# Kernel optimization log

Measured on AMD Instinct MI355X. Metric: run time of the kernel, lower is better.

Reference implementation:

```python
import jax, jax.numpy as jnp
import numpy as np

N = 50000   # nodes
F = 128     # v_feats
K = 128     # filters
H = 3       # multi_head
M = 10      # fixed neighbor count (hardcoded repeat(1,10,1) in source)


def setup_inputs() -> dict:
    key = jax.random.key(0)
    ks = jax.random.split(key, 10)
    vertices = jax.random.normal(ks[0], (N, F), jnp.float32)
    nh_indices = jax.random.randint(ks[1], (N, M), 0, N)
    int_indices = jax.random.randint(ks[2], (N, M), 0, N)
    nh_edges = jax.random.uniform(ks[3], (N, M), jnp.float32)
    int_edges = jax.random.uniform(ks[4], (N, M), jnp.float32)
    is_int = jax.random.randint(ks[5], (N,), 0, 2)
    scale = 0.05
    Wvc = jax.random.normal(ks[6], (H, F, K), jnp.float32) * scale
    Wvn_int = jax.random.normal(ks[7], (H, F, K), jnp.float32) * scale
    Wvn_nh = jax.random.normal(ks[8], (H, F, K), jnp.float32) * scale
    a = jax.random.normal(ks[9], (H, 2 * K, 1), jnp.float32) * scale
    bv = jnp.zeros((H, K), jnp.float32)
    return dict(vertices=vertices, nh_indices=nh_indices, int_indices=int_indices,
                nh_edges=nh_edges, int_edges=int_edges, is_int=is_int,
                Wvc=Wvc, bv=bv, Wvn_int=Wvn_int, Wvn_nh=Wvn_nh, a=a)


def reference(vertices, nh_indices, int_indices, nh_edges, int_edges, is_int,
              Wvc, bv, Wvn_int, Wvn_nh, a):
    n = vertices.shape[0]
    k = a.shape[1] // 2
    # Project center and neighbor features for all heads at once.
    Zc = jnp.einsum('nf,hfk->hnk', vertices, Wvc)        # [H,N,K]
    Vint = jnp.einsum('nf,hfk->hnk', vertices, Wvn_int)  # [H,N,K]
    Vnh = jnp.einsum('nf,hfk->hnk', vertices, Wvn_nh)    # [H,N,K]
    # cat((neighbor, center)) @ a  ==  neighbor @ a[:k] + center @ a[k:]
    a_n = a[:, :k, 0]  # [H,K]
    a_c = a[:, k:, 0]  # [H,K]
    e_center = jnp.einsum('hnk,hk->hn', Zc, a_c)[:, :, None]  # [H,N,1]

    def branch(Vside, idx, edges):
        mask = (idx != -1).astype(vertices.dtype)           # [N,M], -1 = pad
        g = Vside[:, idx]                                   # [H,N,M,K] gather
        e = jnp.einsum('hnmk,hk->hnm', g, a_n) + e_center   # [H,N,M]
        # faithful to source: scores zeroed (not -inf) by mask/edges before softmax
        e = e * mask[None] * edges[None]
        alpha = jax.nn.softmax(e, axis=2)                   # [H,N,M]
        norm = jnp.maximum(mask.sum(axis=1), 1.0)           # [N]
        Zn = jnp.einsum('hnmk,hnm->hnk', g * mask[None, :, :, None], alpha)
        return Zn / norm[None, :, None]

    Zn_inter = branch(Vint, int_indices, int_edges)
    Zn_chain = branch(Vnh, nh_indices, nh_edges)
    z = jax.nn.relu(Zc + Zn_inter + Zn_chain + bv[:, None, :])  # [H,N,K]
    # torch.cat(head outputs, dim=1) -> [N, H*K]
    return jnp.transpose(z, (1, 0, 2)).reshape(n, -1)
```

## Files before the change

kernel.cpp:

```cpp
#include <hip/hip_runtime.h>
#include <stdint.h>

#define N_V 50000
#define F_DIM 128
#define K_DIM 128
#define H_DIM 3
#define M_DIM 10
#define TILES_PER_BLK 4

using bf16x8 = __attribute__((ext_vector_type(8))) short;
using f32x4  = __attribute__((ext_vector_type(4))) float;

__device__ inline unsigned short f2bf(float f) {
    union { float f; uint32_t u; } v; v.f = f;
    uint32_t u = v.u;
    u += 0x7fffu + ((u >> 16) & 1u);
    return (unsigned short)(u >> 16);
}

#define LDS_AS __attribute__((address_space(3)))
__device__ inline void gl2lds16(const void* g, void* l) {
    __builtin_amdgcn_global_load_lds(
        (const __attribute__((address_space(1))) unsigned int*)g,
        (LDS_AS unsigned int*)l, 16, 0, 0);
}

#define WTOT (9 * 128 * 128)
#define XCH  (N_V * 16)
#define WACT (9 * 128)

__global__ void prep(const float* __restrict__ Wvc,
                     const float* __restrict__ Wvn_int,
                     const float* __restrict__ Wvn_nh,
                     const float* __restrict__ X,
                     const float* __restrict__ a,
                     unsigned short* __restrict__ Wt,
                     unsigned short* __restrict__ Xb,
                     unsigned short* __restrict__ wab) {
    int idx = blockIdx.x * 256 + threadIdx.x;
    if (idx < WTOT) {
        int b   = idx >> 14;
        int rem = idx & 16383;
        int k = rem >> 7;
        int f = rem & 127;
        int h = b / 3, t = b - 3 * h;
        const float* src = (t == 0) ? Wvc : (t == 1) ? Wvn_int : Wvn_nh;
        Wt[idx] = f2bf(src[(h * 128 + f) * 128 + k]);
        return;
    }
    int xi = idx - WTOT;
    if (xi < XCH) {
        const float4* Xv = (const float4*)X;
        float4 v0 = Xv[xi * 2];
        float4 v1 = Xv[xi * 2 + 1];
        uint4 o;
        o.x = (uint32_t)f2bf(v0.x) | ((uint32_t)f2bf(v0.y) << 16);
        o.y = (uint32_t)f2bf(v0.z) | ((uint32_t)f2bf(v0.w) << 16);
        o.z = (uint32_t)f2bf(v1.x) | ((uint32_t)f2bf(v1.y) << 16);
        o.w = (uint32_t)f2bf(v1.z) | ((uint32_t)f2bf(v1.w) << 16);
        *(uint4*)&Xb[(size_t)xi * 8] = o;
        return;
    }
    int wi = xi - XCH;
    if (wi < WACT) {
        int b = wi >> 7, f = wi & 127;
        int h = b / 3, t = b - 3 * h;
        const float* src = (t == 0) ? Wvc : (t == 1) ? Wvn_int : Wvn_nh;
        const float4* wrow = (const float4*)&src[(h * 128 + f) * 128];
        const float4* av   = (const float4*)&a[h * 256 + (t == 0 ? 128 : 0)];
        float acc = 0.f;
        #pragma unroll 8
        for (int c = 0; c < 32; ++c) {
            float4 w = wrow[c], x = av[c];
            acc += w.x * x.x + w.y * x.y + w.z * x.z + w.w * x.w;
        }
        wab[b * 128 + f] = f2bf(acc);
    }
}

__global__ __launch_bounds__(256, 3) void gemm_kernel(
    const unsigned short* __restrict__ Xb,
    const unsigned short* __restrict__ Wt,
    const unsigned short* __restrict__ wab,
    float* __restrict__ out,
    uint8_t* __restrict__ Vint,
    uint8_t* __restrict__ Vnh,
    float* __restrict__ ec4,
    float* __restrict__ ei4,
    float* __restrict__ en4) {
    __shared__ unsigned short As[2][64 * 128];

    const int tid  = threadIdx.x;
    const int b    = blockIdx.y;
    const int hh   = b / 3;
    const int tt   = b - 3 * hh;
    const int wv   = tid >> 6;
    const int lane = tid & 63;
    const int q    = lane >> 4;
    const int ln   = lane & 15;
    const int cb   = (wv >> 1) * 64;
    const int rb   = (wv & 1) * 32;
    const int m0   = blockIdx.x * (64 * TILES_PER_BLK);

    auto stage = [&](int buf, int tile) {
        const int mb = m0 + tile * 64;
        #pragma unroll
        for (int it = 0; it < 4; ++it) {
            int c16 = it * 256 + tid;
            int r   = c16 >> 4;
            int p   = c16 & 15;
            int lch = p ^ (r & 15);
            int gr  = mb + r;
            if (gr >= N_V) gr = 0;
            gl2lds16(Xb + (size_t)gr * 128 + lch * 8, &As[buf][c16 * 8]);
        }
    };

    stage(0, 0);

    const unsigned short* Wb = Wt + (size_t)b * 16384;
    bf16x8 bfr[4][4];
    #pragma unroll
    for (int ct = 0; ct < 4; ++ct) {
        int col = cb + 4 * ln + ct;
        #pragma unroll
        for (int kk = 0; kk < 4; ++kk)
            bfr[ct][kk] = *(const bf16x8*)&Wb[col * 128 + kk * 32 + q * 8];
    }

    const bool do_e = (b == 0) && (wv < 2);
    bf16x8 wz[4];
    if (do_e) {
        #pragma unroll
        for (int kk = 0; kk < 4; ++kk) {
            bf16x8 z = {0, 0, 0, 0, 0, 0, 0, 0};
            if (ln < 9) z = *(const bf16x8*)&wab[ln * 128 + kk * 32 + q * 8];
            wz[kk] = z;
        }
    }

    __syncthreads();

    const int c0 = cb + 4 * ln;
    #pragma unroll
    for (int t = 0; t < TILES_PER_BLK; ++t) {
        const int mb = m0 + t * 64;

        if (t + 1 < TILES_PER_BLK) stage((t + 1) & 1, t + 1);

        bf16x8 afr[2][4];
        #pragma unroll
        for (int rt = 0; rt < 2; ++rt) {
            int r = rb + rt * 16 + ln;
            #pragma unroll
            for (int kk = 0; kk < 4; ++kk) {
                int p = (kk * 4 + q) ^ ln;
                afr[rt][kk] = *(const bf16x8*)&As[t & 1][r * 128 + p * 8];
            }
        }

        f32x4 acc[2][4];
        #pragma unroll
        for (int rt = 0; rt < 2; ++rt)
            #pragma unroll
            for (int ct = 0; ct < 4; ++ct) acc[rt][ct] = (f32x4){0.f, 0.f, 0.f, 0.f};

        #pragma unroll
        for (int rt = 0; rt < 2; ++rt)
            #pragma unroll
            for (int kk = 0; kk < 4; ++kk)
                #pragma unroll
                for (int ct = 0; ct < 4; ++ct)
                    acc[rt][ct] = __builtin_amdgcn_mfma_f32_16x16x32_bf16(
                        afr[rt][kk], bfr[ct][kk], acc[rt][ct], 0, 0, 0);

        if (do_e) {
            #pragma unroll
            for (int rt = 0; rt < 2; ++rt) {
                f32x4 ae = (f32x4){0.f, 0.f, 0.f, 0.f};
                #pragma unroll
                for (int kk = 0; kk < 4; ++kk)
                    ae = __builtin_amdgcn_mfma_f32_16x16x32_bf16(
                        afr[rt][kk], wz[kk], ae, 0, 0, 0);
                if (ln < 9) {
                    int h2 = ln / 3, t2 = ln - 3 * h2;
                    float* ep = (t2 == 0) ? ec4 : (t2 == 1) ? ei4 : en4;
                    #pragma unroll
                    for (int rg = 0; rg < 4; ++rg) {
                        int gr = mb + rb + rt * 16 + q * 4 + rg;
                        if (gr < N_V) ep[gr * 4 + h2] = ae[rg];
                    }
                }
            }
        }

        __syncthreads();

        if (tt == 0) {
            #pragma unroll
            for (int rt = 0; rt < 2; ++rt)
                #pragma unroll
                for (int rg = 0; rg < 4; ++rg) {
                    int gr = mb + rb + rt * 16 + q * 4 + rg;
                    if (gr >= N_V) continue;
                    float4 v = make_float4(acc[rt][0][rg], acc[rt][1][rg],
                                           acc[rt][2][rg], acc[rt][3][rg]);
                    *(float4*)&out[(size_t)gr * 384 + hh * 128 + c0] = v;
                }
        } else {
            uint8_t* Vside = (tt == 1) ? Vint : Vnh;
            #pragma unroll
            for (int rt = 0; rt < 2; ++rt)
                #pragma unroll
                for (int rg = 0; rg < 4; ++rg) {
                    int gr = mb + rb + rt * 16 + q * 4 + rg;
                    if (gr >= N_V) continue;
                    int pk = __builtin_amdgcn_cvt_pk_fp8_f32(
                        acc[rt][0][rg], acc[rt][1][rg], 0, false);
                    pk = __builtin_amdgcn_cvt_pk_fp8_f32(
                        acc[rt][2][rg], acc[rt][3][rg], pk, true);
                    *(uint32_t*)&Vside[((size_t)(hh * N_V + gr)) * 128 + c0] =
                        (uint32_t)pk;
                }
        }
    }
}

__global__ __launch_bounds__(256) void attn_kernel(
    const int* __restrict__ nh_idx, const int* __restrict__ int_idx,
    const float* __restrict__ nh_edge, const float* __restrict__ int_edge,
    const float* __restrict__ bv,
    const uint8_t* __restrict__ Vint,
    const uint8_t* __restrict__ Vnh,
    const float* __restrict__ ec4, const float* __restrict__ ei4,
    const float* __restrict__ en4,
    float* __restrict__ out) {
    const int wv   = threadIdx.x >> 6;
    const int lane = threadIdx.x & 63;
    const int n    = blockIdx.x * 4 + wv;
    if (n >= N_V) return;
    const int g  = lane >> 4;
    const int gl = lane & 15;

    const bool part = (g <= 1) && (gl < M_DIM);
    int jm = -1; float wm = 0.f;
    if (part) {
        const int*   idx = (g == 0) ? int_idx  : nh_idx;
        const float* ed  = (g == 0) ? int_edge : nh_edge;
        jm = idx[n * M_DIM + gl];
        wm = ed[n * M_DIM + gl];
    }
    const bool  valid = part && (jm >= 0);
    const int   jc    = valid ? jm : 0;
    const float vfl   = valid ? 1.f : 0.f;

    float cf = vfl;
    #pragma unroll
    for (int off = 1; off < 16; off <<= 1) cf += __shfl_xor(cf, off, 64);
    const float cnorm = fmaxf(cf, 1.f);

    const int src_base = (g < 2 ? 0 : 16) + (g & 1) * 5;
    int jrow[5];
    #pragma unroll
    for (int i = 0; i < 5; ++i) jrow[i] = __shfl(jc, src_base + i, 64);

    uint2 pv[3][5];
    #pragma unroll
    for (int h = 0; h < H_DIM; ++h) {
        const uint8_t* Vb = ((g < 2) ? Vint : Vnh) + (size_t)h * N_V * 128;
        #pragma unroll
        for (int i = 0; i < 5; ++i)
            pv[h][i] = *(const uint2*)&Vb[(size_t)jrow[i] * 128 + gl * 8];
    }
    float4 ev = make_float4(0.f, 0.f, 0.f, 0.f);
    if (part) ev = *(const float4*)&(((g == 0) ? ei4 : en4)[jc * 4]);
    const float4 ecv = *(const float4*)&ec4[n * 4];

    float4 zc[3], bb[3];
    if (g < 2) {
        #pragma unroll
        for (int h = 0; h < H_DIM; ++h) {
            zc[h] = *(const float4*)&out[(size_t)n * 384 + h * 128 + gl * 8 + g * 4];
            bb[h] = *(const float4*)&bv[h * 128 + gl * 8 + g * 4];
        }
    }

    #pragma unroll
    for (int h = 0; h < H_DIM; ++h) {
        const float eh  = (h == 0) ? ev.x  : (h == 1) ? ev.y  : ev.z;
        const float ech = (h == 0) ? ecv.x : (h == 1) ? ecv.y : ecv.z;

        float l = -3.0e38f;
        if (part) l = valid ? (eh + ech) * wm : 0.f;
        float mx = l;
        #pragma unroll
        for (int off = 1; off < 16; off <<= 1) mx = fmaxf(mx, __shfl_xor(mx, off, 64));
        float ex = part ? __expf(l - mx) : 0.f;
        float sv = ex;
        #pragma unroll
        for (int off = 1; off < 16; off <<= 1) sv += __shfl_xor(sv, off, 64);
        float alphap = valid ? ex / (sv * cnorm) : 0.f;

        float acc[8] = {0.f, 0.f, 0.f, 0.f, 0.f, 0.f, 0.f, 0.f};
        #pragma unroll
        for (int i = 0; i < 5; ++i) {
            float al = __shfl(alphap, src_base + i, 64);
            uint2 p  = pv[h][i];
            auto f01 = __builtin_amdgcn_cvt_pk_f32_fp8(p.x, false);
            auto f23 = __builtin_amdgcn_cvt_pk_f32_fp8(p.x, true);
            auto f45 = __builtin_amdgcn_cvt_pk_f32_fp8(p.y, false);
            auto f67 = __builtin_amdgcn_cvt_pk_f32_fp8(p.y, true);
            acc[0] += al * f01[0];
            acc[1] += al * f01[1];
            acc[2] += al * f23[0];
            acc[3] += al * f23[1];
            acc[4] += al * f45[0];
            acc[5] += al * f45[1];
            acc[6] += al * f67[0];
            acc[7] += al * f67[1];
        }
        #pragma unroll
        for (int c = 0; c < 8; ++c) {
            acc[c] += __shfl_xor(acc[c], 16, 64);
            acc[c] += __shfl_xor(acc[c], 32, 64);
        }
        if (g < 2) {
            size_t o = (size_t)n * 384 + h * 128 + gl * 8 + g * 4;
            float4 zn;
            if (g == 0) zn = make_float4(acc[0], acc[1], acc[2], acc[3]);
            else        zn = make_float4(acc[4], acc[5], acc[6], acc[7]);
            float4 r;
            r.x = fmaxf(zc[h].x + zn.x + bb[h].x, 0.f);
            r.y = fmaxf(zc[h].y + zn.y + bb[h].y, 0.f);
            r.z = fmaxf(zc[h].z + zn.z + bb[h].z, 0.f);
            r.w = fmaxf(zc[h].w + zn.w + bb[h].w, 0.f);
            *(float4*)&out[o] = r;
        }
    }
}

extern "C" void kernel_launch(void* const* d_in, const int* in_sizes, int n_in,
                              void* d_out, int out_size, void* d_ws, size_t ws_size,
                              hipStream_t stream) {
    const float* vertices    = (const float*)d_in[0];
    const int*   nh_indices  = (const int*)d_in[1];
    const int*   int_indices = (const int*)d_in[2];
    const float* nh_edges    = (const float*)d_in[3];
    const float* int_edges   = (const float*)d_in[4];
    const float* Wvc     = (const float*)d_in[6];
    const float* bv      = (const float*)d_in[7];
    const float* Wvn_int = (const float*)d_in[8];
    const float* Wvn_nh  = (const float*)d_in[9];
    const float* a       = (const float*)d_in[10];
    float* out = (float*)d_out;

    char* ws = (char*)d_ws;
    size_t off = 0;
    unsigned short* Wt = (unsigned short*)(ws + off);
    off += (size_t)WTOT * 2;                  off = (off + 255) & ~(size_t)255;
    unsigned short* wab = (unsigned short*)(ws + off);
    off += (size_t)WACT * 2;                  off = (off + 255) & ~(size_t)255;
    unsigned short* Xb = (unsigned short*)(ws + off);
    off += (size_t)N_V * 128 * 2;             off = (off + 255) & ~(size_t)255;
    uint8_t* Vint = (uint8_t*)(ws + off);
    off += (size_t)H_DIM * N_V * 128;         off = (off + 255) & ~(size_t)255;
    uint8_t* Vnh = (uint8_t*)(ws + off);
    off += (size_t)H_DIM * N_V * 128;         off = (off + 255) & ~(size_t)255;
    float* ec4 = (float*)(ws + off);
    off += (size_t)N_V * 4 * 4;               off = (off + 255) & ~(size_t)255;
    float* ei4 = (float*)(ws + off);
    off += (size_t)N_V * 4 * 4;               off = (off + 255) & ~(size_t)255;
    float* en4 = (float*)(ws + off);
    off += (size_t)N_V * 4 * 4;

    int prep_threads = WTOT + XCH + WACT;
    prep<<<(prep_threads + 255) / 256, 256, 0, stream>>>(
        Wvc, Wvn_int, Wvn_nh, vertices, a, Wt, Xb, wab);

    dim3 grid_g((N_V + 64 * TILES_PER_BLK - 1) / (64 * TILES_PER_BLK), 9);
    gemm_kernel<<<grid_g, 256, 0, stream>>>(Xb, Wt, wab, out, Vint, Vnh,
                                            ec4, ei4, en4);

    attn_kernel<<<(N_V + 3) / 4, 256, 0, stream>>>(
        nh_indices, int_indices, nh_edges, int_edges, bv,
        Vint, Vnh, ec4, ei4, en4, out);
}
```

Before: 246.1 us.

## Store center projection in fp16, interleave heads in V layout, drop softmax max

The GEMM now writes the center projection Zc to a separate fp16 buffer instead of fp32 into the output, which halves the write and later read traffic. The fp8 neighbor projections switch to a node-major layout with all three heads contiguous, so each gathered neighbor row is one 384-byte region instead of three scattered rows. The softmax max-subtraction reduction is removed, relying on the small logit range. Risks are lower precision for Zc and possible overflow of exp if the logits grow.

```diff
diff --git a/kernel.cpp b/kernel.cpp
--- a/kernel.cpp
+++ b/kernel.cpp
@@ -10,12 +10,19 @@
 
 using bf16x8 = __attribute__((ext_vector_type(8))) short;
 using f32x4  = __attribute__((ext_vector_type(4))) float;
+using h4     = __attribute__((ext_vector_type(4))) _Float16;
 
 __device__ inline unsigned short f2bf(float f) {
     union { float f; uint32_t u; } v; v.f = f;
     uint32_t u = v.u;
     u += 0x7fffu + ((u >> 16) & 1u);
     return (unsigned short)(u >> 16);
+}
+
+__device__ inline uint32_t pkh2(float a, float b) {
+    union { _Float16 h[2]; uint32_t u; } v;
+    v.h[0] = (_Float16)a; v.h[1] = (_Float16)b;
+    return v.u;
 }
 
 #define LDS_AS __attribute__((address_space(3)))
@@ -82,7 +89,7 @@
     const unsigned short* __restrict__ Xb,
     const unsigned short* __restrict__ Wt,
     const unsigned short* __restrict__ wab,
-    float* __restrict__ out,
+    _Float16* __restrict__ zc16,
     uint8_t* __restrict__ Vint,
     uint8_t* __restrict__ Vnh,
     float* __restrict__ ec4,
@@ -203,9 +210,10 @@
                 for (int rg = 0; rg < 4; ++rg) {
                     int gr = mb + rb + rt * 16 + q * 4 + rg;
                     if (gr >= N_V) continue;
-                    float4 v = make_float4(acc[rt][0][rg], acc[rt][1][rg],
-                                           acc[rt][2][rg], acc[rt][3][rg]);
-                    *(float4*)&out[(size_t)gr * 384 + hh * 128 + c0] = v;
+                    uint2 s;
+                    s.x = pkh2(acc[rt][0][rg], acc[rt][1][rg]);
+                    s.y = pkh2(acc[rt][2][rg], acc[rt][3][rg]);
+                    *(uint2*)&zc16[(size_t)gr * 384 + hh * 128 + c0] = s;
                 }
         } else {
             uint8_t* Vside = (tt == 1) ? Vint : Vnh;
@@ -219,7 +227,7 @@
                         acc[rt][0][rg], acc[rt][1][rg], 0, false);
                     pk = __builtin_amdgcn_cvt_pk_fp8_f32(
                         acc[rt][2][rg], acc[rt][3][rg], pk, true);
-                    *(uint32_t*)&Vside[((size_t)(hh * N_V + gr)) * 128 + c0] =
+                    *(uint32_t*)&Vside[((size_t)gr * 3 + hh) * 128 + c0] =
                         (uint32_t)pk;
                 }
         }
@@ -234,6 +242,7 @@
     const uint8_t* __restrict__ Vnh,
     const float* __restrict__ ec4, const float* __restrict__ ei4,
     const float* __restrict__ en4,
+    const _Float16* __restrict__ zc16,
     float* __restrict__ out) {
     const int wv   = threadIdx.x >> 6;
     const int lane = threadIdx.x & 63;
@@ -264,13 +273,14 @@
     #pragma unroll
     for (int i = 0; i < 5; ++i) jrow[i] = __shfl(jc, src_base + i, 64);
 
+    const uint8_t* Vb = (g < 2) ? Vint : Vnh;
     uint2 pv[3][5];
     #pragma unroll
-    for (int h = 0; h < H_DIM; ++h) {
-        const uint8_t* Vb = ((g < 2) ? Vint : Vnh) + (size_t)h * N_V * 128;
-        #pragma unroll
-        for (int i = 0; i < 5; ++i)
-            pv[h][i] = *(const uint2*)&Vb[(size_t)jrow[i] * 128 + gl * 8];
+    for (int i = 0; i < 5; ++i) {
+        const uint8_t* base = Vb + (size_t)jrow[i] * 384 + gl * 8;
+        #pragma unroll
+        for (int h = 0; h < H_DIM; ++h)
+            pv[h][i] = *(const uint2*)(base + h * 128);
     }
     float4 ev = make_float4(0.f, 0.f, 0.f, 0.f);
     if (part) ev = *(const float4*)&(((g == 0) ? ei4 : en4)[jc * 4]);
@@ -280,7 +290,8 @@
     if (g < 2) {
         #pragma unroll
         for (int h = 0; h < H_DIM; ++h) {
-            zc[h] = *(const float4*)&out[(size_t)n * 384 + h * 128 + gl * 8 + g * 4];
+            h4 z = *(const h4*)&zc16[(size_t)n * 384 + h * 128 + gl * 8 + g * 4];
+            zc[h] = make_float4((float)z[0], (float)z[1], (float)z[2], (float)z[3]);
             bb[h] = *(const float4*)&bv[h * 128 + gl * 8 + g * 4];
         }
     }
@@ -290,12 +301,8 @@
         const float eh  = (h == 0) ? ev.x  : (h == 1) ? ev.y  : ev.z;
         const float ech = (h == 0) ? ecv.x : (h == 1) ? ecv.y : ecv.z;
 
-        float l = -3.0e38f;
-        if (part) l = valid ? (eh + ech) * wm : 0.f;
-        float mx = l;
-        #pragma unroll
-        for (int off = 1; off < 16; off <<= 1) mx = fmaxf(mx, __shfl_xor(mx, off, 64));
-        float ex = part ? __expf(l - mx) : 0.f;
+        float l = (part && valid) ? (eh + ech) * wm : 0.f;
+        float ex = part ? __expf(l) : 0.f;
         float sv = ex;
         #pragma unroll
         for (int off = 1; off < 16; off <<= 1) sv += __shfl_xor(sv, off, 64);
@@ -366,6 +373,8 @@
     off += (size_t)H_DIM * N_V * 128;         off = (off + 255) & ~(size_t)255;
     uint8_t* Vnh = (uint8_t*)(ws + off);
     off += (size_t)H_DIM * N_V * 128;         off = (off + 255) & ~(size_t)255;
+    _Float16* zc16 = (_Float16*)(ws + off);
+    off += (size_t)N_V * 384 * 2;             off = (off + 255) & ~(size_t)255;
     float* ec4 = (float*)(ws + off);
     off += (size_t)N_V * 4 * 4;               off = (off + 255) & ~(size_t)255;
     float* ei4 = (float*)(ws + off);
@@ -378,10 +387,10 @@
         Wvc, Wvn_int, Wvn_nh, vertices, a, Wt, Xb, wab);
 
     dim3 grid_g((N_V + 64 * TILES_PER_BLK - 1) / (64 * TILES_PER_BLK), 9);
-    gemm_kernel<<<grid_g, 256, 0, stream>>>(Xb, Wt, wab, out, Vint, Vnh,
+    gemm_kernel<<<grid_g, 256, 0, stream>>>(Xb, Wt, wab, zc16, Vint, Vnh,
                                             ec4, ei4, en4);
 
     attn_kernel<<<(N_V + 3) / 4, 256, 0, stream>>>(
         nh_indices, int_indices, nh_edges, int_edges, bv,
-        Vint, Vnh, ec4, ei4, en4, out);
-}
+        Vint, Vnh, ec4, ei4, en4, zc16, out);
+}
```

Result: faster. 230.3 us (-6.4%).
